# Performance work log

Measured on AMD Instinct MI355X. Metric: run time of the kernel, lower is better.

## Reference

```python
import jax, jax.numpy as jnp
import numpy as np

N = 50000   # nodes
E = 800000  # edges
F = 128     # num_features
H = 128     # embedding_size
C = 10      # num_classes
G = 64      # graphs in batch


def setup_inputs() -> dict:
    key = jax.random.key(0)
    ks = jax.random.split(key, 12)
    x = jax.random.normal(ks[0], (N, F), dtype=jnp.float32)
    edge_index = jax.random.randint(ks[1], (2, E), 0, N, dtype=jnp.int32)
    batch_index = jnp.sort(jax.random.randint(ks[2], (N,), 0, G, dtype=jnp.int32))

    def lin(k, fan_in, fan_out):
        s = 1.0 / np.sqrt(fan_in)
        kw, kb = jax.random.split(k)
        W = jax.random.uniform(kw, (fan_in, fan_out), jnp.float32, -s, s)
        b = jax.random.uniform(kb, (fan_out,), jnp.float32, -s, s)
        return W, b

    W0, b0 = lin(ks[3], F, H)
    W1, b1 = lin(ks[4], H, H)
    W2, b2 = lin(ks[5], H, H)
    Wa, ba = lin(ks[6], 2 * H, C)
    return {"x": x, "edge_index": edge_index, "batch_index": batch_index,
            "W0": W0, "b0": b0, "W1": W1, "b1": b1, "W2": W2, "b2": b2,
            "Wa": Wa, "ba": ba}


def gcn_conv(x, src, dst, inv_sqrt_deg, W, b):
    # PyG GCNConv: h = x @ W; out_i = sum_{j->i} h_j / sqrt(d_j d_i)
    # with added self loops (deg already includes +1; self-loop term = h_i / d_i).
    h = x @ W                                             # [N, H]
    coef = inv_sqrt_deg[src] * inv_sqrt_deg[dst]          # [E]
    msg = coef[:, None] * h[src]                          # [E, H]
    agg = jax.ops.segment_sum(msg, dst, num_segments=N)   # [N, H]
    agg = agg + (inv_sqrt_deg * inv_sqrt_deg)[:, None] * h  # self loops
    return agg + b


def reference(x, edge_index, batch_index, W0, b0, W1, b1, W2, b2, Wa, ba):
    src, dst = edge_index[0], edge_index[1]
    # degree including self loop
    deg = jax.ops.segment_sum(jnp.ones((E,), x.dtype), dst, num_segments=N) + 1.0
    inv_sqrt_deg = jax.lax.rsqrt(deg)

    h = jax.nn.relu(gcn_conv(x, src, dst, inv_sqrt_deg, W0, b0))
    h = jax.nn.relu(gcn_conv(h, src, dst, inv_sqrt_deg, W1, b1))
    h = jax.nn.relu(gcn_conv(h, src, dst, inv_sqrt_deg, W2, b2))

    counts = jax.ops.segment_sum(jnp.ones((N,), x.dtype), batch_index, num_segments=G)
    sums = jax.ops.segment_sum(h, batch_index, num_segments=G)
    mean = sums / jnp.maximum(counts, 1.0)[:, None]
    mx = jax.ops.segment_max(h, batch_index, num_segments=G)
    mx = jnp.where(counts[:, None] > 0, mx, 0.0)

    aggr = jnp.concatenate([mean, mx], axis=1)            # [G, 2H]
    out = aggr @ Wa + ba                                  # [G, C]
    return out, aggr
```

## Files before the change

kernel.cpp:

```cpp
#include <hip/hip_runtime.h>
#include <stdint.h>

#define N_NODES 50000
#define N_EDGES 800000
#define HID 128
#define NCLS 10
#define NGRAPH 64
#define CAP 64

typedef unsigned short ushort_t;
typedef __attribute__((ext_vector_type(8))) short bf16x8;
typedef __attribute__((ext_vector_type(4))) float f32x4;
typedef __attribute__((ext_vector_type(4))) _Float16 f16x4;
typedef __attribute__((ext_vector_type(8))) _Float16 f16x8;

__device__ __forceinline__ ushort_t f2bf(float f) {
    union { float f; unsigned int i; } v; v.f = f;
    unsigned int u = v.i;
    return (ushort_t)((u + 0x7FFFu + ((u >> 16) & 1u)) >> 16);
}
__device__ __forceinline__ float bf2f(ushort_t u) {
    union { unsigned int i; float f; } v; v.i = ((unsigned int)u) << 16; return v.f;
}
__device__ __forceinline__ int exhi(int p) { return (p >> 16) & 0xffff; }
__device__ __forceinline__ int exlo(int p) { return p & 0xffff; }
__device__ __forceinline__ void add4h(float4& a, f16x4 v) {
    a.x += (float)v[0];
    a.y += (float)v[1];
    a.z += (float)v[2];
    a.w += (float)v[3];
}

__global__ void k_zero(int* cnt, float* sums, float* maxs,
                       const int* __restrict__ batch, int* bound, int* counts,
                       const float* __restrict__ W0, const float* __restrict__ W1,
                       const float* __restrict__ W2, ushort_t* Whi, ushort_t* Wlo) {
    int b = blockIdx.x, t = threadIdx.x;
    if (b < 196) {
        int i = b * 256 + t;
        if (i < N_NODES) cnt[i] = 0;
        if (i < NGRAPH * HID) { sums[i] = 0.f; maxs[i] = 0.f; }
    } else if (b == 196) {
        int g = t;
        if (g <= NGRAPH) {
            int lo = 0, hi = N_NODES;
            while (lo < hi) {
                int mid = (lo + hi) >> 1;
                if (batch[mid] < g) lo = mid + 1; else hi = mid;
            }
            bound[g] = lo;
        }
        __syncthreads();
        if (g < NGRAPH) counts[g] = bound[g + 1] - bound[g];
    } else {
        int gid = (b - 197) * 256 + t;
        int l = gid / (32 * 512);
        int rem = gid - l * 32 * 512;
        int tile = rem >> 9;
        int p = rem & 511;
        int lane = p >> 3, j = p & 7;
        int kk = tile >> 3, c = tile & 7;
        int k = 32 * kk + (lane >> 4) * 8 + j;
        int n = 16 * c + (lane & 15);
        const float* W = (l == 0) ? W0 : (l == 1) ? W1 : W2;
        float x = W[k * 128 + n];
        ushort_t hi = f2bf(x);
        ushort_t lo = f2bf(x - bf2f(hi));
        Whi[l * 16384 + rem] = hi;
        Wlo[l * 16384 + rem] = lo;
    }
}

__global__ void k_fill(const int* __restrict__ src, const int* __restrict__ dst,
                       int* cnt, ushort_t* csr16) {
    int base = (blockIdx.x * 256 + threadIdx.x) * 8;
    if (base + 7 < N_EDGES) {
        int4 da = *(const int4*)(dst + base);
        int4 db = *(const int4*)(dst + base + 4);
        int4 sa = *(const int4*)(src + base);
        int4 sb = *(const int4*)(src + base + 4);
        int p0 = atomicAdd(&cnt[da.x], 1);
        int p1 = atomicAdd(&cnt[da.y], 1);
        int p2 = atomicAdd(&cnt[da.z], 1);
        int p3 = atomicAdd(&cnt[da.w], 1);
        int p4 = atomicAdd(&cnt[db.x], 1);
        int p5 = atomicAdd(&cnt[db.y], 1);
        int p6 = atomicAdd(&cnt[db.z], 1);
        int p7 = atomicAdd(&cnt[db.w], 1);
        if (p0 < CAP) csr16[da.x * CAP + p0] = (ushort_t)sa.x;
        if (p1 < CAP) csr16[da.y * CAP + p1] = (ushort_t)sa.y;
        if (p2 < CAP) csr16[da.z * CAP + p2] = (ushort_t)sa.z;
        if (p3 < CAP) csr16[da.w * CAP + p3] = (ushort_t)sa.w;
        if (p4 < CAP) csr16[db.x * CAP + p4] = (ushort_t)sb.x;
        if (p5 < CAP) csr16[db.y * CAP + p5] = (ushort_t)sb.y;
        if (p6 < CAP) csr16[db.z * CAP + p6] = (ushort_t)sb.z;
        if (p7 < CAP) csr16[db.w * CAP + p7] = (ushort_t)sb.w;
    } else {
        for (int i = base; i < N_EDGES; i++) {
            int d = dst[i];
            int slot = atomicAdd(&cnt[d], 1);
            if (slot < CAP) csr16[d * CAP + slot] = (ushort_t)src[i];
        }
    }
}

__global__ void k_cvt(const float* __restrict__ x, const int* __restrict__ cnt,
                      _Float16* __restrict__ X16) {
    int gid = blockIdx.x * 256 + threadIdx.x;
    int i = gid >> 4, seg = gid & 15;
    float isd = rsqrtf((float)cnt[i] + 1.0f);
    const f32x4* px = (const f32x4*)(x + (size_t)i * HID + seg * 8);
    f32x4 a = px[0], b = px[1];
    f16x8 o;
    o[0] = (_Float16)(isd * a.x); o[1] = (_Float16)(isd * a.y);
    o[2] = (_Float16)(isd * a.z); o[3] = (_Float16)(isd * a.w);
    o[4] = (_Float16)(isd * b.x); o[5] = (_Float16)(isd * b.y);
    o[6] = (_Float16)(isd * b.z); o[7] = (_Float16)(isd * b.w);
    *(f16x8*)(X16 + (size_t)i * HID + seg * 8) = o;
}

__global__ void k_layer(const _Float16* __restrict__ In,
                        const ushort_t* __restrict__ csr16, const int* __restrict__ cnt,
                        const ushort_t* __restrict__ Whi, const ushort_t* __restrict__ Wlo,
                        const float* __restrict__ bias, int scale_out,
                        int pool, const int* __restrict__ batch,
                        float* sums, float* maxs, _Float16* __restrict__ Out) {
    __shared__ float T[16][132];
    __shared__ int sg[16];
    int t = threadIdx.x, wv = t >> 6, lane = t & 63;
    int hl = lane & 31, q = lane >> 5;
    if (pool && t < 16) sg[t] = batch[blockIdx.x * 16 + t];

    for (int r = 0; r < 4; r++) {
        int i = blockIdx.x * 16 + wv * 4 + r;
        int ci = cnt[i];
        int m = min(ci, CAP);
        float isdi = rsqrtf((float)ci + 1.0f);
        int packed = ((const int*)(csr16 + (size_t)i * CAP))[hl];
        float4 a0 = make_float4(0.f, 0.f, 0.f, 0.f);
        float4 a1 = a0, a2 = a0, a3 = a0;
        if (q == 0) {
            f16x4 sv = *(const f16x4*)(In + (size_t)i * HID + hl * 4);
            add4h(a0, sv);
        }
        int e = 0;
        for (; e + 7 < m; e += 8) {
            int k0 = e >> 1;
            int p0 = __shfl(packed, k0);
            int p1 = __shfl(packed, k0 + 1);
            int p2 = __shfl(packed, k0 + 2);
            int p3 = __shfl(packed, k0 + 3);
            int s0 = q ? exhi(p0) : exlo(p0);
            int s1 = q ? exhi(p1) : exlo(p1);
            int s2 = q ? exhi(p2) : exlo(p2);
            int s3 = q ? exhi(p3) : exlo(p3);
            f16x4 v0 = *(const f16x4*)(In + (size_t)s0 * HID + hl * 4);
            f16x4 v1 = *(const f16x4*)(In + (size_t)s1 * HID + hl * 4);
            f16x4 v2 = *(const f16x4*)(In + (size_t)s2 * HID + hl * 4);
            f16x4 v3 = *(const f16x4*)(In + (size_t)s3 * HID + hl * 4);
            add4h(a0, v0); add4h(a1, v1); add4h(a2, v2); add4h(a3, v3);
        }
        for (; e + 1 < m; e += 2) {
            int p = __shfl(packed, e >> 1);
            int s0 = q ? exhi(p) : exlo(p);
            f16x4 v0 = *(const f16x4*)(In + (size_t)s0 * HID + hl * 4);
            add4h(a0, v0);
        }
        if (e < m && q == 0) {
            int p = __shfl(packed, e >> 1);
            int s0 = exlo(p);
            f16x4 v0 = *(const f16x4*)(In + (size_t)s0 * HID + hl * 4);
            add4h(a0, v0);
        }
        float4 s4;
        s4.x = (a0.x + a1.x) + (a2.x + a3.x);
        s4.y = (a0.y + a1.y) + (a2.y + a3.y);
        s4.z = (a0.z + a1.z) + (a2.z + a3.z);
        s4.w = (a0.w + a1.w) + (a2.w + a3.w);
        s4.x += __shfl_xor(s4.x, 32);
        s4.y += __shfl_xor(s4.y, 32);
        s4.z += __shfl_xor(s4.z, 32);
        s4.w += __shfl_xor(s4.w, 32);
        if (q == 0) {
            float4 o;
            o.x = isdi * s4.x; o.y = isdi * s4.y;
            o.z = isdi * s4.z; o.w = isdi * s4.w;
            *(float4*)&T[wv * 4 + r][hl * 4] = o;
        }
    }
    __syncthreads();

    int mrow = lane & 15, qq = lane >> 4;
    f32x4 acc[2];
    acc[0] = (f32x4){0.f, 0.f, 0.f, 0.f};
    acc[1] = (f32x4){0.f, 0.f, 0.f, 0.f};
#pragma unroll
    for (int kk = 0; kk < 4; kk++) {
        const float* tp = &T[mrow][kk * 32 + qq * 8];
        float4 p0 = *(const float4*)tp;
        float4 p1 = *(const float4*)(tp + 4);
        float av[8] = {p0.x, p0.y, p0.z, p0.w, p1.x, p1.y, p1.z, p1.w};
        bf16x8 ahi, alo;
#pragma unroll
        for (int j = 0; j < 8; j++) {
            ushort_t hbits = f2bf(av[j]);
            ahi[j] = (short)hbits;
            alo[j] = (short)f2bf(av[j] - bf2f(hbits));
        }
#pragma unroll
        for (int cl = 0; cl < 2; cl++) {
            int c = wv * 2 + cl;
            const bf16x8 bhi = *(const bf16x8*)(Whi + (((kk * 8 + c) * 64 + lane) << 3));
            const bf16x8 blo = *(const bf16x8*)(Wlo + (((kk * 8 + c) * 64 + lane) << 3));
            acc[cl] = __builtin_amdgcn_mfma_f32_16x16x32_bf16(ahi, bhi, acc[cl], 0, 0, 0);
            acc[cl] = __builtin_amdgcn_mfma_f32_16x16x32_bf16(alo, bhi, acc[cl], 0, 0, 0);
            acc[cl] = __builtin_amdgcn_mfma_f32_16x16x32_bf16(ahi, blo, acc[cl], 0, 0, 0);
        }
    }
    int rb = blockIdx.x * 16 + qq * 4;
    if (!pool) {
        float osc[4];
#pragma unroll
        for (int rr = 0; rr < 4; rr++)
            osc[rr] = scale_out ? rsqrtf((float)cnt[rb + rr] + 1.0f) : 1.0f;
#pragma unroll
        for (int cl = 0; cl < 2; cl++) {
            int col = (wv * 2 + cl) * 16 + mrow;
            float bcol = bias[col];
#pragma unroll
            for (int rr = 0; rr < 4; rr++) {
                float val = fmaxf(acc[cl][rr] + bcol, 0.f);
                Out[(size_t)(rb + rr) * HID + col] = (_Float16)(val * osc[rr]);
            }
        }
    } else {
        __syncthreads();
#pragma unroll
        for (int cl = 0; cl < 2; cl++) {
            int col = (wv * 2 + cl) * 16 + mrow;
            float bcol = bias[col];
#pragma unroll
            for (int rr = 0; rr < 4; rr++)
                T[qq * 4 + rr][col] = fmaxf(acc[cl][rr] + bcol, 0.f);
        }
        __syncthreads();
        int f = t & 127, half = t >> 7;
        int cur = sg[0];
        float s = 0.f, mx = 0.f;
        for (int r = 0; r < 16; r++) {
            int g = sg[r];
            if (g != cur) {
                if (half == 0) atomicAdd(&sums[cur * HID + f], s);
                else atomicMax((int*)&maxs[cur * HID + f], __float_as_int(mx));
                s = 0.f; mx = 0.f; cur = g;
            }
            float v = T[r][f];
            s += v;
            mx = fmaxf(mx, v);
        }
        if (half == 0) atomicAdd(&sums[cur * HID + f], s);
        else atomicMax((int*)&maxs[cur * HID + f], __float_as_int(mx));
    }
}

__global__ void k_final(const float* __restrict__ sums, const float* __restrict__ maxs,
                        const int* __restrict__ counts, const float* __restrict__ Wa,
                        const float* __restrict__ ba, float* __restrict__ out) {
    __shared__ float a[256];
    __shared__ float red[4];
    int g = blockIdx.x, t = threadIdx.x;
    float denom = fmaxf((float)counts[g], 1.f);
    float val = (t < 128) ? (sums[g * HID + t] / denom) : maxs[g * HID + (t - 128)];
    a[t] = val;
    out[NGRAPH * NCLS + g * 256 + t] = val;
    __syncthreads();
    for (int c = 0; c < NCLS; c++) {
        float p = a[t] * Wa[t * NCLS + c];
        for (int o = 32; o > 0; o >>= 1) p += __shfl_down(p, o);
        if ((t & 63) == 0) red[t >> 6] = p;
        __syncthreads();
        if (t == 0) {
            out[g * NCLS + c] = red[0] + red[1] + red[2] + red[3] + ba[c];
        }
        __syncthreads();
    }
}

extern "C" void kernel_launch(void* const* d_in, const int* in_sizes, int n_in,
                              void* d_out, int out_size, void* d_ws, size_t ws_size,
                              hipStream_t stream) {
    const float* x = (const float*)d_in[0];
    const int* ei = (const int*)d_in[1];
    const int* src = ei;
    const int* dst = ei + N_EDGES;
    const int* batch = (const int*)d_in[2];
    const float* W0 = (const float*)d_in[3];
    const float* b0 = (const float*)d_in[4];
    const float* W1 = (const float*)d_in[5];
    const float* b1 = (const float*)d_in[6];
    const float* W2 = (const float*)d_in[7];
    const float* b2 = (const float*)d_in[8];
    const float* Wa = (const float*)d_in[9];
    const float* ba = (const float*)d_in[10];
    float* out = (float*)d_out;

    char* ws = (char*)d_ws;
    int*       cnt    = (int*)(ws + 0);
    int*       bound  = (int*)(ws + 200192);
    int*       counts = (int*)(ws + 200576);
    float*     sums   = (float*)(ws + 200832);
    float*     maxs   = (float*)(ws + 233600);
    ushort_t*  Whi    = (ushort_t*)(ws + 266368);
    ushort_t*  Wlo    = (ushort_t*)(ws + 364672);
    ushort_t*  csr16  = (ushort_t*)(ws + 462976);
    _Float16*  X16    = (_Float16*)(ws + 7462976);
    _Float16*  hA     = (_Float16*)(ws + 20262976);
    _Float16*  hB     = (_Float16*)(ws + 33062976);

    k_zero<<<389, 256, 0, stream>>>(cnt, sums, maxs, batch, bound, counts,
                                    W0, W1, W2, Whi, Wlo);
    k_fill<<<391, 256, 0, stream>>>(src, dst, cnt, csr16);
    k_cvt<<<3125, 256, 0, stream>>>(x, cnt, X16);

    k_layer<<<3125, 256, 0, stream>>>(X16, csr16, cnt, Whi, Wlo, b0, 1,
                                      0, batch, sums, maxs, hA);
    k_layer<<<3125, 256, 0, stream>>>(hA, csr16, cnt, Whi + 16384, Wlo + 16384, b1, 1,
                                      0, batch, sums, maxs, hB);
    k_layer<<<3125, 256, 0, stream>>>(hB, csr16, cnt, Whi + 32768, Wlo + 32768, b2, 0,
                                      1, batch, sums, maxs, hA);

    k_final<<<NGRAPH, 256, 0, stream>>>(sums, maxs, counts, Wa, ba, out);
}
```

Before: 271.9 us.

## Fuse CSR fill into prep kernel, memset workspace, load CSR directly in gather

Replaces the zeroing kernel with a hipMemsetAsync and merges the edge-bucketing fill into the prep kernel that also computes graph bounds and splits the weights, removing one launch. In the layer gather loop, neighbour indices are now read as int4 straight from the CSR row instead of being broadcast with wave shuffles. Four neighbour rows are summed in fp16 before being added to a single fp32 accumulator, which cuts the accumulator registers but gives up some precision and ILP.

```diff
diff --git a/kernel.cpp b/kernel.cpp
--- a/kernel.cpp
+++ b/kernel.cpp
@@ -31,16 +31,43 @@
     a.w += (float)v[3];
 }
 
-__global__ void k_zero(int* cnt, float* sums, float* maxs,
+__global__ void k_prep(const int* __restrict__ src, const int* __restrict__ dst,
+                       int* cnt, ushort_t* csr16,
                        const int* __restrict__ batch, int* bound, int* counts,
                        const float* __restrict__ W0, const float* __restrict__ W1,
                        const float* __restrict__ W2, ushort_t* Whi, ushort_t* Wlo) {
     int b = blockIdx.x, t = threadIdx.x;
-    if (b < 196) {
-        int i = b * 256 + t;
-        if (i < N_NODES) cnt[i] = 0;
-        if (i < NGRAPH * HID) { sums[i] = 0.f; maxs[i] = 0.f; }
-    } else if (b == 196) {
+    if (b < 391) {
+        int base = (b * 256 + t) * 8;
+        if (base + 7 < N_EDGES) {
+            int4 da = *(const int4*)(dst + base);
+            int4 db = *(const int4*)(dst + base + 4);
+            int4 sa = *(const int4*)(src + base);
+            int4 sb = *(const int4*)(src + base + 4);
+            int p0 = atomicAdd(&cnt[da.x], 1);
+            int p1 = atomicAdd(&cnt[da.y], 1);
+            int p2 = atomicAdd(&cnt[da.z], 1);
+            int p3 = atomicAdd(&cnt[da.w], 1);
+            int p4 = atomicAdd(&cnt[db.x], 1);
+            int p5 = atomicAdd(&cnt[db.y], 1);
+            int p6 = atomicAdd(&cnt[db.z], 1);
+            int p7 = atomicAdd(&cnt[db.w], 1);
+            if (p0 < CAP) csr16[da.x * CAP + p0] = (ushort_t)sa.x;
+            if (p1 < CAP) csr16[da.y * CAP + p1] = (ushort_t)sa.y;
+            if (p2 < CAP) csr16[da.z * CAP + p2] = (ushort_t)sa.z;
+            if (p3 < CAP) csr16[da.w * CAP + p3] = (ushort_t)sa.w;
+            if (p4 < CAP) csr16[db.x * CAP + p4] = (ushort_t)sb.x;
+            if (p5 < CAP) csr16[db.y * CAP + p5] = (ushort_t)sb.y;
+            if (p6 < CAP) csr16[db.z * CAP + p6] = (ushort_t)sb.z;
+            if (p7 < CAP) csr16[db.w * CAP + p7] = (ushort_t)sb.w;
+        } else {
+            for (int i = base; i < N_EDGES; i++) {
+                int d = dst[i];
+                int slot = atomicAdd(&cnt[d], 1);
+                if (slot < CAP) csr16[d * CAP + slot] = (ushort_t)src[i];
+            }
+        }
+    } else if (b == 391) {
         int g = t;
         if (g <= NGRAPH) {
             int lo = 0, hi = N_NODES;
@@ -53,7 +80,7 @@
         __syncthreads();
         if (g < NGRAPH) counts[g] = bound[g + 1] - bound[g];
     } else {
-        int gid = (b - 197) * 256 + t;
+        int gid = (b - 392) * 256 + t;
         int l = gid / (32 * 512);
         int rem = gid - l * 32 * 512;
         int tile = rem >> 9;
@@ -71,39 +98,6 @@
     }
 }
 
-__global__ void k_fill(const int* __restrict__ src, const int* __restrict__ dst,
-                       int* cnt, ushort_t* csr16) {
-    int base = (blockIdx.x * 256 + threadIdx.x) * 8;
-    if (base + 7 < N_EDGES) {
-        int4 da = *(const int4*)(dst + base);
-        int4 db = *(const int4*)(dst + base + 4);
-        int4 sa = *(const int4*)(src + base);
-        int4 sb = *(const int4*)(src + base + 4);
-        int p0 = atomicAdd(&cnt[da.x], 1);
-        int p1 = atomicAdd(&cnt[da.y], 1);
-        int p2 = atomicAdd(&cnt[da.z], 1);
-        int p3 = atomicAdd(&cnt[da.w], 1);
-        int p4 = atomicAdd(&cnt[db.x], 1);
-        int p5 = atomicAdd(&cnt[db.y], 1);
-        int p6 = atomicAdd(&cnt[db.z], 1);
-        int p7 = atomicAdd(&cnt[db.w], 1);
-        if (p0 < CAP) csr16[da.x * CAP + p0] = (ushort_t)sa.x;
-        if (p1 < CAP) csr16[da.y * CAP + p1] = (ushort_t)sa.y;
-        if (p2 < CAP) csr16[da.z * CAP + p2] = (ushort_t)sa.z;
-        if (p3 < CAP) csr16[da.w * CAP + p3] = (ushort_t)sa.w;
-        if (p4 < CAP) csr16[db.x * CAP + p4] = (ushort_t)sb.x;
-        if (p5 < CAP) csr16[db.y * CAP + p5] = (ushort_t)sb.y;
-        if (p6 < CAP) csr16[db.z * CAP + p6] = (ushort_t)sb.z;
-        if (p7 < CAP) csr16[db.w * CAP + p7] = (ushort_t)sb.w;
-    } else {
-        for (int i = base; i < N_EDGES; i++) {
-            int d = dst[i];
-            int slot = atomicAdd(&cnt[d], 1);
-            if (slot < CAP) csr16[d * CAP + slot] = (ushort_t)src[i];
-        }
-    }
-}
-
 __global__ void k_cvt(const float* __restrict__ x, const int* __restrict__ cnt,
                       _Float16* __restrict__ X16) {
     int gid = blockIdx.x * 256 + threadIdx.x;
@@ -136,9 +130,9 @@
         int ci = cnt[i];
         int m = min(ci, CAP);
         float isdi = rsqrtf((float)ci + 1.0f);
-        int packed = ((const int*)(csr16 + (size_t)i * CAP))[hl];
+        const int* crow = (const int*)(csr16 + (size_t)i * CAP);
         float4 a0 = make_float4(0.f, 0.f, 0.f, 0.f);
-        float4 a1 = a0, a2 = a0, a3 = a0;
+        float4 a1 = a0;
         if (q == 0) {
             f16x4 sv = *(const f16x4*)(In + (size_t)i * HID + hl * 4);
             add4h(a0, sv);
@@ -146,37 +140,35 @@
         int e = 0;
         for (; e + 7 < m; e += 8) {
             int k0 = e >> 1;
-            int p0 = __shfl(packed, k0);
-            int p1 = __shfl(packed, k0 + 1);
-            int p2 = __shfl(packed, k0 + 2);
-            int p3 = __shfl(packed, k0 + 3);
-            int s0 = q ? exhi(p0) : exlo(p0);
-            int s1 = q ? exhi(p1) : exlo(p1);
-            int s2 = q ? exhi(p2) : exlo(p2);
-            int s3 = q ? exhi(p3) : exlo(p3);
+            int4 pk = *(const int4*)(crow + k0);
+            int s0 = q ? exhi(pk.x) : exlo(pk.x);
+            int s1 = q ? exhi(pk.y) : exlo(pk.y);
+            int s2 = q ? exhi(pk.z) : exlo(pk.z);
+            int s3 = q ? exhi(pk.w) : exlo(pk.w);
             f16x4 v0 = *(const f16x4*)(In + (size_t)s0 * HID + hl * 4);
             f16x4 v1 = *(const f16x4*)(In + (size_t)s1 * HID + hl * 4);
             f16x4 v2 = *(const f16x4*)(In + (size_t)s2 * HID + hl * 4);
             f16x4 v3 = *(const f16x4*)(In + (size_t)s3 * HID + hl * 4);
-            add4h(a0, v0); add4h(a1, v1); add4h(a2, v2); add4h(a3, v3);
+            f16x4 u = (v0 + v1) + (v2 + v3);
+            add4h(a1, u);
         }
         for (; e + 1 < m; e += 2) {
-            int p = __shfl(packed, e >> 1);
+            int p = crow[e >> 1];
             int s0 = q ? exhi(p) : exlo(p);
             f16x4 v0 = *(const f16x4*)(In + (size_t)s0 * HID + hl * 4);
             add4h(a0, v0);
         }
         if (e < m && q == 0) {
-            int p = __shfl(packed, e >> 1);
+            int p = crow[e >> 1];
             int s0 = exlo(p);
             f16x4 v0 = *(const f16x4*)(In + (size_t)s0 * HID + hl * 4);
             add4h(a0, v0);
         }
         float4 s4;
-        s4.x = (a0.x + a1.x) + (a2.x + a3.x);
-        s4.y = (a0.y + a1.y) + (a2.y + a3.y);
-        s4.z = (a0.z + a1.z) + (a2.z + a3.z);
-        s4.w = (a0.w + a1.w) + (a2.w + a3.w);
+        s4.x = a0.x + a1.x;
+        s4.y = a0.y + a1.y;
+        s4.z = a0.z + a1.z;
+        s4.w = a0.w + a1.w;
         s4.x += __shfl_xor(s4.x, 32);
         s4.y += __shfl_xor(s4.y, 32);
         s4.z += __shfl_xor(s4.z, 32);
@@ -317,9 +309,9 @@
     _Float16*  hA     = (_Float16*)(ws + 20262976);
     _Float16*  hB     = (_Float16*)(ws + 33062976);
 
-    k_zero<<<389, 256, 0, stream>>>(cnt, sums, maxs, batch, bound, counts,
+    hipMemsetAsync(ws, 0, 266368, stream);
+    k_prep<<<584, 256, 0, stream>>>(src, dst, cnt, csr16, batch, bound, counts,
                                     W0, W1, W2, Whi, Wlo);
-    k_fill<<<391, 256, 0, stream>>>(src, dst, cnt, csr16);
     k_cvt<<<3125, 256, 0, stream>>>(x, cnt, X16);
 
     k_layer<<<3125, 256, 0, stream>>>(X16, csr16, cnt, Whi, Wlo, b0, 1,
```

Result: slower. 281.2 us (+3.4%).

## Merge zero/fill kernels via memset and unroll edge gather to 16

Applied to the files above, without the earlier changes.

Zeroing of the count, sum and max buffers is replaced by a hipMemsetAsync over the workspace prefix. CSR fill, graph-boundary search and weight splitting are merged into a single prep kernel, which removes one launch. The layer kernel gains a 16-edge unrolled gather loop so more independent loads are in flight per iteration, at the cost of higher register pressure. The memset still needs its own stream operation, so launch savings may be small.

```diff
diff --git a/kernel.cpp b/kernel.cpp
--- a/kernel.cpp
+++ b/kernel.cpp
@@ -31,16 +31,43 @@
     a.w += (float)v[3];
 }
 
-__global__ void k_zero(int* cnt, float* sums, float* maxs,
+__global__ void k_prep(const int* __restrict__ src, const int* __restrict__ dst,
+                       int* cnt, ushort_t* csr16,
                        const int* __restrict__ batch, int* bound, int* counts,
                        const float* __restrict__ W0, const float* __restrict__ W1,
                        const float* __restrict__ W2, ushort_t* Whi, ushort_t* Wlo) {
     int b = blockIdx.x, t = threadIdx.x;
-    if (b < 196) {
-        int i = b * 256 + t;
-        if (i < N_NODES) cnt[i] = 0;
-        if (i < NGRAPH * HID) { sums[i] = 0.f; maxs[i] = 0.f; }
-    } else if (b == 196) {
+    if (b < 391) {
+        int base = (b * 256 + t) * 8;
+        if (base + 7 < N_EDGES) {
+            int4 da = *(const int4*)(dst + base);
+            int4 db = *(const int4*)(dst + base + 4);
+            int4 sa = *(const int4*)(src + base);
+            int4 sb = *(const int4*)(src + base + 4);
+            int p0 = atomicAdd(&cnt[da.x], 1);
+            int p1 = atomicAdd(&cnt[da.y], 1);
+            int p2 = atomicAdd(&cnt[da.z], 1);
+            int p3 = atomicAdd(&cnt[da.w], 1);
+            int p4 = atomicAdd(&cnt[db.x], 1);
+            int p5 = atomicAdd(&cnt[db.y], 1);
+            int p6 = atomicAdd(&cnt[db.z], 1);
+            int p7 = atomicAdd(&cnt[db.w], 1);
+            if (p0 < CAP) csr16[da.x * CAP + p0] = (ushort_t)sa.x;
+            if (p1 < CAP) csr16[da.y * CAP + p1] = (ushort_t)sa.y;
+            if (p2 < CAP) csr16[da.z * CAP + p2] = (ushort_t)sa.z;
+            if (p3 < CAP) csr16[da.w * CAP + p3] = (ushort_t)sa.w;
+            if (p4 < CAP) csr16[db.x * CAP + p4] = (ushort_t)sb.x;
+            if (p5 < CAP) csr16[db.y * CAP + p5] = (ushort_t)sb.y;
+            if (p6 < CAP) csr16[db.z * CAP + p6] = (ushort_t)sb.z;
+            if (p7 < CAP) csr16[db.w * CAP + p7] = (ushort_t)sb.w;
+        } else {
+            for (int i = base; i < N_EDGES; i++) {
+                int d = dst[i];
+                int slot = atomicAdd(&cnt[d], 1);
+                if (slot < CAP) csr16[d * CAP + slot] = (ushort_t)src[i];
+            }
+        }
+    } else if (b == 391) {
         int g = t;
         if (g <= NGRAPH) {
             int lo = 0, hi = N_NODES;
@@ -53,7 +80,7 @@
         __syncthreads();
         if (g < NGRAPH) counts[g] = bound[g + 1] - bound[g];
     } else {
-        int gid = (b - 197) * 256 + t;
+        int gid = (b - 392) * 256 + t;
         int l = gid / (32 * 512);
         int rem = gid - l * 32 * 512;
         int tile = rem >> 9;
@@ -71,39 +98,6 @@
     }
 }
 
-__global__ void k_fill(const int* __restrict__ src, const int* __restrict__ dst,
-                       int* cnt, ushort_t* csr16) {
-    int base = (blockIdx.x * 256 + threadIdx.x) * 8;
-    if (base + 7 < N_EDGES) {
-        int4 da = *(const int4*)(dst + base);
-        int4 db = *(const int4*)(dst + base + 4);
-        int4 sa = *(const int4*)(src + base);
-        int4 sb = *(const int4*)(src + base + 4);
-        int p0 = atomicAdd(&cnt[da.x], 1);
-        int p1 = atomicAdd(&cnt[da.y], 1);
-        int p2 = atomicAdd(&cnt[da.z], 1);
-        int p3 = atomicAdd(&cnt[da.w], 1);
-        int p4 = atomicAdd(&cnt[db.x], 1);
-        int p5 = atomicAdd(&cnt[db.y], 1);
-        int p6 = atomicAdd(&cnt[db.z], 1);
-        int p7 = atomicAdd(&cnt[db.w], 1);
-        if (p0 < CAP) csr16[da.x * CAP + p0] = (ushort_t)sa.x;
-        if (p1 < CAP) csr16[da.y * CAP + p1] = (ushort_t)sa.y;
-        if (p2 < CAP) csr16[da.z * CAP + p2] = (ushort_t)sa.z;
-        if (p3 < CAP) csr16[da.w * CAP + p3] = (ushort_t)sa.w;
-        if (p4 < CAP) csr16[db.x * CAP + p4] = (ushort_t)sb.x;
-        if (p5 < CAP) csr16[db.y * CAP + p5] = (ushort_t)sb.y;
-        if (p6 < CAP) csr16[db.z * CAP + p6] = (ushort_t)sb.z;
-        if (p7 < CAP) csr16[db.w * CAP + p7] = (ushort_t)sb.w;
-    } else {
-        for (int i = base; i < N_EDGES; i++) {
-            int d = dst[i];
-            int slot = atomicAdd(&cnt[d], 1);
-            if (slot < CAP) csr16[d * CAP + slot] = (ushort_t)src[i];
-        }
-    }
-}
-
 __global__ void k_cvt(const float* __restrict__ x, const int* __restrict__ cnt,
                       _Float16* __restrict__ X16) {
     int gid = blockIdx.x * 256 + threadIdx.x;
@@ -144,6 +138,35 @@
             add4h(a0, sv);
         }
         int e = 0;
+        for (; e + 15 < m; e += 16) {
+            int k0 = e >> 1;
+            int p0 = __shfl(packed, k0);
+            int p1 = __shfl(packed, k0 + 1);
+            int p2 = __shfl(packed, k0 + 2);
+            int p3 = __shfl(packed, k0 + 3);
+            int p4 = __shfl(packed, k0 + 4);
+            int p5 = __shfl(packed, k0 + 5);
+            int p6 = __shfl(packed, k0 + 6);
+            int p7 = __shfl(packed, k0 + 7);
+            int s0 = q ? exhi(p0) : exlo(p0);
+            int s1 = q ? exhi(p1) : exlo(p1);
+            int s2 = q ? exhi(p2) : exlo(p2);
+            int s3 = q ? exhi(p3) : exlo(p3);
+            int s4 = q ? exhi(p4) : exlo(p4);
+            int s5 = q ? exhi(p5) : exlo(p5);
+            int s6 = q ? exhi(p6) : exlo(p6);
+            int s7 = q ? exhi(p7) : exlo(p7);
+            f16x4 v0 = *(const f16x4*)(In + (size_t)s0 * HID + hl * 4);
+            f16x4 v1 = *(const f16x4*)(In + (size_t)s1 * HID + hl * 4);
+            f16x4 v2 = *(const f16x4*)(In + (size_t)s2 * HID + hl * 4);
+            f16x4 v3 = *(const f16x4*)(In + (size_t)s3 * HID + hl * 4);
+            f16x4 v4 = *(const f16x4*)(In + (size_t)s4 * HID + hl * 4);
+            f16x4 v5 = *(const f16x4*)(In + (size_t)s5 * HID + hl * 4);
+            f16x4 v6 = *(const f16x4*)(In + (size_t)s6 * HID + hl * 4);
+            f16x4 v7 = *(const f16x4*)(In + (size_t)s7 * HID + hl * 4);
+            add4h(a0, v0); add4h(a1, v1); add4h(a2, v2); add4h(a3, v3);
+            add4h(a0, v4); add4h(a1, v5); add4h(a2, v6); add4h(a3, v7);
+        }
         for (; e + 7 < m; e += 8) {
             int k0 = e >> 1;
             int p0 = __shfl(packed, k0);
@@ -317,9 +340,9 @@
     _Float16*  hA     = (_Float16*)(ws + 20262976);
     _Float16*  hB     = (_Float16*)(ws + 33062976);
 
-    k_zero<<<389, 256, 0, stream>>>(cnt, sums, maxs, batch, bound, counts,
+    hipMemsetAsync(ws, 0, 266368, stream);
+    k_prep<<<584, 256, 0, stream>>>(src, dst, cnt, csr16, batch, bound, counts,
                                     W0, W1, W2, Whi, Wlo);
-    k_fill<<<391, 256, 0, stream>>>(src, dst, cnt, csr16);
     k_cvt<<<3125, 256, 0, stream>>>(x, cnt, X16);
 
     k_layer<<<3125, 256, 0, stream>>>(X16, csr16, cnt, Whi, Wlo, b0, 1,
```

After: 270.2 us (median of 2 runs). Within noise of the previous version (-0.6%).
